# Kernel optimization log

Hardware: AMD Instinct MI355X
Metric: run time of the kernel (lower is better)

The kernel has to match this reference:

```python
import jax, jax.numpy as jnp
import numpy as np

DIM = 768
HEADS = 12

def setup_inputs() -> dict:
    key = jax.random.key(0)
    k_x, k_qw, k_qb, k_pw, k_pb = jax.random.split(key, 5)
    x = jax.random.normal(k_x, (4, 2048, DIM), dtype=jnp.float32)
    s = 1.0 / np.sqrt(DIM)
    # torch nn.Linear convention: y = x @ W.T + b, W shape [out, in]
    qkv_w = jax.random.uniform(k_qw, (3 * DIM, DIM), jnp.float32, -s, s)
    qkv_b = jax.random.uniform(k_qb, (3 * DIM,), jnp.float32, -s, s)
    proj_w = jax.random.uniform(k_pw, (DIM, DIM), jnp.float32, -s, s)
    proj_b = jax.random.uniform(k_pb, (DIM,), jnp.float32, -s, s)
    return {"x": x, "qkv_w": qkv_w, "qkv_b": qkv_b, "proj_w": proj_w, "proj_b": proj_b}

def reference(x, qkv_w, qkv_b, proj_w, proj_b):
    B, N, C = x.shape
    H = HEADS
    D = C // H
    scale = D ** -0.5
    qkv = x @ qkv_w.T + qkv_b                      # [B, N, 3C]
    qkv = qkv.reshape(B, N, 3, H, D).transpose(2, 0, 3, 1, 4)  # [3, B, H, N, D]
    q, k, v = qkv[0], qkv[1], qkv[2]
    attn = jnp.einsum('bhnd,bhmd->bhnm', q, k) * scale  # [B, H, N, N]
    attn = jax.nn.softmax(attn, axis=-1)           # dropout p=0.0 -> identity
    out = jnp.einsum('bhnm,bhmd->bhnd', attn, v)   # [B, H, N, D]
    out = out.transpose(0, 2, 1, 3).reshape(B, N, C)
    return out @ proj_w.T + proj_b
```

## Files before the change

kernel.cpp:

```cpp
#include <hip/hip_runtime.h>

#define DIM 768
#define HEADS 12
#define HDIM 64
#define BATCH 4
#define SEQ 2048
#define QSCALE 0.1803368787f
#define MFIX 16.0f
#define QKVSZ ((size_t)BATCH * HEADS * SEQ * HDIM)

typedef __bf16 bf16x8 __attribute__((ext_vector_type(8)));
typedef float  f32x4  __attribute__((ext_vector_type(4)));
typedef float  f32x16 __attribute__((ext_vector_type(16)));
typedef unsigned short u16x8 __attribute__((ext_vector_type(8)));
typedef unsigned short ushort_t;

__device__ inline float exp2_hw(float x){
    float r;
    asm("v_exp_f32 %0, %1\n\ts_nop 0" : "=v"(r) : "v"(x));
    return r;
}
__device__ inline unsigned short f2bf(float x){
    unsigned int u = __float_as_uint(x);
    u += 0x7fffu + ((u >> 16) & 1u);
    return (unsigned short)(u >> 16);
}
__device__ inline unsigned int cvtpk(float lo, float hi){
    unsigned int r;
    asm("v_cvt_pk_bf16_f32 %0, %1, %2" : "=v"(r) : "v"(lo), "v"(hi));
    return r;
}
__device__ inline void gload_lds16(const void* g, void* lds) {
    __builtin_amdgcn_global_load_lds(
        (const __attribute__((address_space(1))) void*)g,
        (__attribute__((address_space(3))) void*)lds, 16, 0, 0);
}

__global__ __launch_bounds__(256) void cvt3(
    const float* __restrict__ s0, ushort_t* __restrict__ d0, int v0,
    const float* __restrict__ s1, ushort_t* __restrict__ d1, int v1,
    const float* __restrict__ s2, ushort_t* __restrict__ d2, int v2)
{
    int idx = blockIdx.x * 256 + threadIdx.x;
    const float* s; ushort_t* d;
    if (idx < v0)           { s = s0; d = d0; }
    else if (idx < v0 + v1) { idx -= v0; s = s1; d = d1; }
    else                    { idx -= v0 + v1; s = s2; d = d2; }
    float4 a = *(const float4*)(s + (size_t)idx * 8);
    float4 b = *(const float4*)(s + (size_t)idx * 8 + 4);
    u16x8 p;
    p[0] = f2bf(a.x); p[1] = f2bf(a.y); p[2] = f2bf(a.z); p[3] = f2bf(a.w);
    p[4] = f2bf(b.x); p[5] = f2bf(b.y); p[6] = f2bf(b.z); p[7] = f2bf(b.w);
    *(u16x8*)(d + (size_t)idx * 8) = p;
}

template <int MODE>
__global__ __launch_bounds__(256) void gemm_mfma(
    const ushort_t* __restrict__ A, const ushort_t* __restrict__ W,
    const float* __restrict__ bias, void* __restrict__ outp,
    int M, int N, int K)
{
    __shared__ ushort_t As[128 * 64];
    __shared__ ushort_t Bs[128 * 64];

    const int tid  = threadIdx.x;
    const int lane = tid & 63;
    const int w    = tid >> 6;
    const int l16  = lane & 15;
    const int lg   = lane >> 4;
    const int wm = w >> 1, wn = w & 1;
    const int m0 = blockIdx.y << 7;
    const int n0 = blockIdx.x << 7;

    const int srow = lane >> 3;
    const int clds = lane & 7;
    const int cg   = clds ^ srow;
    const ushort_t* pA = A + (size_t)(m0 + w * 32 + srow) * K + cg * 8;
    const ushort_t* pB = W + (size_t)(n0 + w * 32 + srow) * K + cg * 8;
    ushort_t* lA = As + (w * 32) * 64;
    ushort_t* lB = Bs + (w * 32) * 64;

    f32x4 acc[4][4];
#pragma unroll
    for (int mi = 0; mi < 4; ++mi)
#pragma unroll
        for (int ni = 0; ni < 4; ++ni) acc[mi][ni] = (f32x4){0.f, 0.f, 0.f, 0.f};

    const int s7  = l16 & 7;
    const int ck0 = (lg ^ s7) << 3;
    const int ck1 = ((4 | lg) ^ s7) << 3;
    const int arow = (wm * 64 + l16) * 64;
    const int brow = (wn * 64 + l16) * 64;

    const int KT = K >> 6;
    for (int kt = 0; kt < KT; ++kt) {
        __syncthreads();
        const ushort_t* ga = pA + kt * 64;
        const ushort_t* gb = pB + kt * 64;
#pragma unroll
        for (int j = 0; j < 4; ++j) {
            gload_lds16(ga + (size_t)j * 8 * K, lA + j * 8 * 64);
            gload_lds16(gb + (size_t)j * 8 * K, lB + j * 8 * 64);
        }
        __syncthreads();

        bf16x8 af[2][4], bfr[2][4];
#pragma unroll
        for (int mi = 0; mi < 4; ++mi) {
            af[0][mi] = *(const bf16x8*)(As + arow + mi * 16 * 64 + ck0);
            af[1][mi] = *(const bf16x8*)(As + arow + mi * 16 * 64 + ck1);
        }
#pragma unroll
        for (int ni = 0; ni < 4; ++ni) {
            bfr[0][ni] = *(const bf16x8*)(Bs + brow + ni * 16 * 64 + ck0);
            bfr[1][ni] = *(const bf16x8*)(Bs + brow + ni * 16 * 64 + ck1);
        }
#pragma unroll
        for (int kk = 0; kk < 2; ++kk)
#pragma unroll
            for (int mi = 0; mi < 4; ++mi)
#pragma unroll
                for (int ni = 0; ni < 4; ++ni)
                    acc[mi][ni] = __builtin_amdgcn_mfma_f32_16x16x32_bf16(
                        af[kk][mi], bfr[kk][ni], acc[mi][ni], 0, 0, 0);
    }

#pragma unroll
    for (int ni = 0; ni < 4; ++ni) {
        const int n = n0 + wn * 64 + ni * 16 + l16;
        const float bv = bias[n];
        if (MODE == 0) {
            float* out = (float*)outp;
#pragma unroll
            for (int mi = 0; mi < 4; ++mi)
#pragma unroll
                for (int r = 0; r < 4; ++r) {
                    const int m = m0 + wm * 64 + mi * 16 + lg * 4 + r;
                    out[(size_t)m * N + n] = acc[mi][ni][r] + bv;
                }
        } else {
            ushort_t* out = (ushort_t*)outp;
            const int which = n / DIM;
            const int rem   = n % DIM;
            const int h = rem >> 6;
            const int d = rem & 63;
            const float sc = (which == 0) ? QSCALE : 1.0f;
            ushort_t* base = out + (size_t)which * QKVSZ;
#pragma unroll
            for (int mi = 0; mi < 4; ++mi)
#pragma unroll
                for (int r = 0; r < 4; ++r) {
                    const int m = m0 + wm * 64 + mi * 16 + lg * 4 + r;
                    const int b = m >> 11;
                    const int nrow = m & (SEQ - 1);
                    base[((size_t)(b * HEADS + h) * SEQ + nrow) * HDIM + d] =
                        f2bf((acc[mi][ni][r] + bv) * sc);
                }
        }
    }
}

__global__ __launch_bounds__(256) void transpose_v(
    const ushort_t* __restrict__ V, ushort_t* __restrict__ VT)
{
    __shared__ ushort_t t[64][65];
    const int tid = threadIdx.x;
    const int bh  = blockIdx.y;
    const int k0  = blockIdx.x << 6;

#pragma unroll
    for (int p = 0; p < 2; ++p) {
        int idx = tid + (p << 8);
        int row = idx >> 3;
        int ch  = idx & 7;
        union { bf16x8 v; ushort_t s[8]; } u;
        u.v = *(const bf16x8*)(V + ((size_t)bh * SEQ + k0 + row) * HDIM + ch * 8);
#pragma unroll
        for (int j = 0; j < 8; ++j) t[row][ch * 8 + j] = u.s[j];
    }
    __syncthreads();
#pragma unroll
    for (int p = 0; p < 2; ++p) {
        int idx = tid + (p << 8);
        int d   = idx >> 3;
        int ch  = idx & 7;
        union { bf16x8 v; ushort_t s[8]; } u;
#pragma unroll
        for (int j = 0; j < 8; ++j) u.s[j] = t[ch * 8 + j][d];
        *(bf16x8*)(VT + ((size_t)bh * HDIM + d) * SEQ + k0 + ch * 8) = u.v;
    }
}

__global__ __launch_bounds__(256) void flash_attn_mfma(
    const ushort_t* __restrict__ Qg, const ushort_t* __restrict__ Kg,
    const ushort_t* __restrict__ VTg, ushort_t* __restrict__ Og)
{
    __shared__ ushort_t Ks[2][64 * 64];
    __shared__ ushort_t Vs[2][64 * 64];

    const int tid  = threadIdx.x;
    const int lane = tid & 63;
    const int w    = tid >> 6;
    const int l32  = lane & 31;
    const int hi   = lane >> 5;

    const int L   = blockIdx.x;
    const int swz = (L & 7) * 96 + (L >> 3);
    const int bh  = swz >> 4;
    const int qt  = swz & 15;
    const int q0  = qt * 128 + w * 32;

    const ushort_t* Qp  = Qg + ((size_t)bh * SEQ + q0) * HDIM;
    const ushort_t* Kp  = Kg + (size_t)bh * SEQ * HDIM;
    const ushort_t* VTp = VTg + (size_t)bh * HDIM * SEQ;

    bf16x8 qf[4];
#pragma unroll
    for (int kd = 0; kd < 4; ++kd)
        qf[kd] = *(const bf16x8*)(Qp + l32 * HDIM + kd * 16 + hi * 8);

    f32x16 oacc[2];
#pragma unroll
    for (int nb = 0; nb < 2; ++nb)
#pragma unroll
        for (int r = 0; r < 16; ++r) oacc[nb][r] = 0.f;
    float lsum = 0.f;

    const int srow = lane >> 3;
    const int clds = lane & 7;
    const int cg   = clds ^ srow;
    const int rw   = w * 16 + srow;

    auto stage = [&](int buf, int kt) {
        ushort_t* lk = Ks[buf] + w * 1024;
        ushort_t* lv = Vs[buf] + w * 1024;
        const ushort_t* gk = Kp + ((size_t)kt * 64 + rw) * HDIM + cg * 8;
        const ushort_t* gv = VTp + (size_t)rw * SEQ + kt * 64 + cg * 8;
#pragma unroll
        for (int j = 0; j < 2; ++j) {
            gload_lds16(gk + j * 8 * HDIM, lk + j * 512);
            gload_lds16(gv + j * 8 * SEQ,  lv + j * 512);
        }
    };

    stage(0, 0);
    __syncthreads();

    int cur = 0;
    const int NT = SEQ / 64;
    for (int kt = 0; kt < NT; ++kt) {
        if (kt + 1 < NT) stage(cur ^ 1, kt + 1);

        const ushort_t* Kb = Ks[cur];
        const ushort_t* Vb = Vs[cur];

#pragma unroll
        for (int b = 0; b < 2; ++b) {
            f32x16 sacc;
#pragma unroll
            for (int r = 0; r < 16; ++r) sacc[r] = 0.f;
            const int arow = b * 32 + l32;
            const int s7   = arow & 7;
            __builtin_amdgcn_s_setprio(1);
#pragma unroll
            for (int kd = 0; kd < 4; ++kd) {
                bf16x8 kf = *(const bf16x8*)(Kb + arow * 64 + (((kd * 2 + hi) ^ s7) << 3));
                sacc = __builtin_amdgcn_mfma_f32_32x32x16_bf16(kf, qf[kd], sacc, 0, 0, 0);
            }
            __builtin_amdgcn_s_setprio(0);

            float p[16];
#pragma unroll
            for (int r = 0; r < 16; ++r) p[r] = exp2_hw(sacc[r] - MFIX);
            float t0 = (p[0] + p[1]) + (p[2] + p[3]);
            float t1 = (p[4] + p[5]) + (p[6] + p[7]);
            float t2 = (p[8] + p[9]) + (p[10] + p[11]);
            float t3 = (p[12] + p[13]) + (p[14] + p[15]);
            lsum += (t0 + t1) + (t2 + t3);

#pragma unroll
            for (int s = 0; s < 2; ++s) {
                unsigned int x0 = cvtpk(p[8 * s + 0], p[8 * s + 1]);
                unsigned int y0 = cvtpk(p[8 * s + 4], p[8 * s + 5]);
                unsigned int x1 = cvtpk(p[8 * s + 2], p[8 * s + 3]);
                unsigned int y1 = cvtpk(p[8 * s + 6], p[8 * s + 7]);
                asm("v_permlane32_swap_b32 %0, %1" : "+v"(x0), "+v"(y0));
                asm("v_permlane32_swap_b32 %0, %1" : "+v"(x1), "+v"(y1));
                union { bf16x8 v; unsigned int w4[4]; } pa;
                pa.w4[0] = x0; pa.w4[1] = x1; pa.w4[2] = y0; pa.w4[3] = y1;
                const int kc = b * 4 + s * 2 + hi;
                __builtin_amdgcn_s_setprio(1);
#pragma unroll
                for (int nb = 0; nb < 2; ++nb) {
                    int d = nb * 32 + l32;
                    bf16x8 vf = *(const bf16x8*)(Vb + d * 64 + ((kc ^ (d & 7)) << 3));
                    oacc[nb] = __builtin_amdgcn_mfma_f32_32x32x16_bf16(
                        pa.v, vf, oacc[nb], 0, 0, 0);
                }
                __builtin_amdgcn_s_setprio(0);
            }
        }

        __syncthreads();
        cur ^= 1;
    }

    lsum += __shfl_xor(lsum, 32);
    float linv = 1.0f / lsum;
    const int b_ = bh / HEADS;
    const int h_ = bh % HEADS;
    ushort_t* Ob = Og + ((size_t)b_ * SEQ + q0) * DIM + h_ * HDIM;
#pragma unroll
    for (int r = 0; r < 16; ++r) {
        int q = (r & 3) + 8 * (r >> 2) + 4 * hi;
        float li = __shfl(linv, q);
#pragma unroll
        for (int nb = 0; nb < 2; ++nb)
            Ob[(size_t)q * DIM + nb * 32 + l32] = f2bf(oacc[nb][r] * li);
    }
}

extern "C" void kernel_launch(void* const* d_in, const int* in_sizes, int n_in,
                              void* d_out, int out_size, void* d_ws, size_t ws_size,
                              hipStream_t stream)
{
    const float* x      = (const float*)d_in[0];
    const float* qkv_w  = (const float*)d_in[1];
    const float* qkv_b  = (const float*)d_in[2];
    const float* proj_w = (const float*)d_in[3];
    const float* proj_b = (const float*)d_in[4];
    float* out = (float*)d_out;

    ushort_t* qb     = (ushort_t*)d_ws;
    ushort_t* kb     = qb + QKVSZ;
    ushort_t* vb     = qb + 2 * QKVSZ;
    ushort_t* vtb    = qb + 3 * QKVSZ;
    ushort_t* attn   = qb + 4 * QKVSZ;
    ushort_t* xb     = qb + 5 * QKVSZ;
    ushort_t* qkvwb  = xb + QKVSZ;
    ushort_t* projwb = qkvwb + (size_t)3 * DIM * DIM;

    const int M = BATCH * SEQ;
    const int NX  = M * DIM;
    const int NQW = 3 * DIM * DIM;
    const int NPW = DIM * DIM;

    cvt3<<<dim3((NX + NQW + NPW) / (8 * 256)), dim3(256), 0, stream>>>(
        x, xb, NX / 8, qkv_w, qkvwb, NQW / 8, proj_w, projwb, NPW / 8);

    dim3 g1(3 * DIM / 128, M / 128);
    gemm_mfma<1><<<g1, dim3(256), 0, stream>>>(xb, qkvwb, qkv_b, (void*)qb, M, 3 * DIM, DIM);

    transpose_v<<<dim3(SEQ / 64, BATCH * HEADS), dim3(256), 0, stream>>>(vb, vtb);

    flash_attn_mfma<<<dim3(768), dim3(256), 0, stream>>>(qb, kb, vtb, attn);

    dim3 g3(DIM / 128, M / 128);
    gemm_mfma<0><<<g3, dim3(256), 0, stream>>>(attn, projwb, proj_b, (void*)out, M, DIM, DIM);
}
```

Baseline: 155.1 us.

## Fuse V transpose into QKV GEMM epilogue and compute row sums via MFMA

The QKV GEMM epilogue now writes V directly in transposed [B,H,D,N] layout using packed 4-element stores, which removes the separate transpose_v kernel and its extra global round trip. In the attention kernel, the softmax row sum is accumulated with an extra MFMA against a ones vector instead of scalar adds and shuffles, and the fixed max offset is folded into the score accumulator's initial value. Staging pointer arithmetic is also simplified to incremental pointers. The price is one more MFMA per P-tile, and the transposed V stores in the GEMM are strided rather than contiguous.

New measurement: 146.4 us, median of 2. 1.06x faster.

```diff
diff --git a/kernel.cpp b/kernel.cpp
--- a/kernel.cpp
+++ b/kernel.cpp
@@ -144,50 +144,35 @@
             const int rem   = n % DIM;
             const int h = rem >> 6;
             const int d = rem & 63;
-            const float sc = (which == 0) ? QSCALE : 1.0f;
-            ushort_t* base = out + (size_t)which * QKVSZ;
-#pragma unroll
-            for (int mi = 0; mi < 4; ++mi)
-#pragma unroll
-                for (int r = 0; r < 4; ++r) {
-                    const int m = m0 + wm * 64 + mi * 16 + lg * 4 + r;
+            if (which < 2) {
+                const float sc = (which == 0) ? QSCALE : 1.0f;
+                ushort_t* base = out + (size_t)which * QKVSZ;
+#pragma unroll
+                for (int mi = 0; mi < 4; ++mi)
+#pragma unroll
+                    for (int r = 0; r < 4; ++r) {
+                        const int m = m0 + wm * 64 + mi * 16 + lg * 4 + r;
+                        const int b = m >> 11;
+                        const int nrow = m & (SEQ - 1);
+                        base[((size_t)(b * HEADS + h) * SEQ + nrow) * HDIM + d] =
+                            f2bf((acc[mi][ni][r] + bv) * sc);
+                    }
+            } else {
+                ushort_t* base = out + 2 * QKVSZ;
+#pragma unroll
+                for (int mi = 0; mi < 4; ++mi) {
+                    const int m = m0 + wm * 64 + mi * 16 + lg * 4;
                     const int b = m >> 11;
                     const int nrow = m & (SEQ - 1);
-                    base[((size_t)(b * HEADS + h) * SEQ + nrow) * HDIM + d] =
-                        f2bf((acc[mi][ni][r] + bv) * sc);
+                    ushort4 pk;
+                    pk.x = f2bf(acc[mi][ni][0] + bv);
+                    pk.y = f2bf(acc[mi][ni][1] + bv);
+                    pk.z = f2bf(acc[mi][ni][2] + bv);
+                    pk.w = f2bf(acc[mi][ni][3] + bv);
+                    *(ushort4*)&base[((size_t)(b * HEADS + h) * HDIM + d) * SEQ + nrow] = pk;
                 }
-        }
-    }
-}
-
-__global__ __launch_bounds__(256) void transpose_v(
-    const ushort_t* __restrict__ V, ushort_t* __restrict__ VT)
-{
-    __shared__ ushort_t t[64][65];
-    const int tid = threadIdx.x;
-    const int bh  = blockIdx.y;
-    const int k0  = blockIdx.x << 6;
-
-#pragma unroll
-    for (int p = 0; p < 2; ++p) {
-        int idx = tid + (p << 8);
-        int row = idx >> 3;
-        int ch  = idx & 7;
-        union { bf16x8 v; ushort_t s[8]; } u;
-        u.v = *(const bf16x8*)(V + ((size_t)bh * SEQ + k0 + row) * HDIM + ch * 8);
-#pragma unroll
-        for (int j = 0; j < 8; ++j) t[row][ch * 8 + j] = u.s[j];
-    }
-    __syncthreads();
-#pragma unroll
-    for (int p = 0; p < 2; ++p) {
-        int idx = tid + (p << 8);
-        int d   = idx >> 3;
-        int ch  = idx & 7;
-        union { bf16x8 v; ushort_t s[8]; } u;
-#pragma unroll
-        for (int j = 0; j < 8; ++j) u.s[j] = t[ch * 8 + j][d];
-        *(bf16x8*)(VT + ((size_t)bh * HDIM + d) * SEQ + k0 + ch * 8) = u.v;
+            }
+        }
     }
 }
 
@@ -195,8 +180,8 @@
     const ushort_t* __restrict__ Qg, const ushort_t* __restrict__ Kg,
     const ushort_t* __restrict__ VTg, ushort_t* __restrict__ Og)
 {
-    __shared__ ushort_t Ks[2][64 * 64];
-    __shared__ ushort_t Vs[2][64 * 64];
+    __shared__ ushort_t Ks[2][4096];
+    __shared__ ushort_t Vs[2][4096];
 
     const int tid  = threadIdx.x;
     const int lane = tid & 63;
@@ -219,48 +204,62 @@
     for (int kd = 0; kd < 4; ++kd)
         qf[kd] = *(const bf16x8*)(Qp + l32 * HDIM + kd * 16 + hi * 8);
 
-    f32x16 oacc[2];
+    bf16x8 ones;
+    {
+        union { bf16x8 v; unsigned int w4[4]; } u;
+        u.w4[0] = u.w4[1] = u.w4[2] = u.w4[3] = 0x3F803F80u;
+        ones = u.v;
+    }
+
+    f32x16 oacc[2], lacc;
 #pragma unroll
     for (int nb = 0; nb < 2; ++nb)
 #pragma unroll
         for (int r = 0; r < 16; ++r) oacc[nb][r] = 0.f;
-    float lsum = 0.f;
+#pragma unroll
+    for (int r = 0; r < 16; ++r) lacc[r] = 0.f;
 
     const int srow = lane >> 3;
     const int clds = lane & 7;
     const int cg   = clds ^ srow;
     const int rw   = w * 16 + srow;
 
-    auto stage = [&](int buf, int kt) {
-        ushort_t* lk = Ks[buf] + w * 1024;
-        ushort_t* lv = Vs[buf] + w * 1024;
-        const ushort_t* gk = Kp + ((size_t)kt * 64 + rw) * HDIM + cg * 8;
-        const ushort_t* gv = VTp + (size_t)rw * SEQ + kt * 64 + cg * 8;
-#pragma unroll
-        for (int j = 0; j < 2; ++j) {
-            gload_lds16(gk + j * 8 * HDIM, lk + j * 512);
-            gload_lds16(gv + j * 8 * SEQ,  lv + j * 512);
-        }
+    const ushort_t* gk = Kp + (size_t)rw * HDIM + cg * 8;
+    const ushort_t* gv = VTp + (size_t)rw * SEQ + cg * 8;
+    ushort_t* lk0 = &Ks[0][0] + w * 1024;
+    ushort_t* lv0 = &Vs[0][0] + w * 1024;
+
+    auto stage = [&](int buf) {
+        ushort_t* lkb = lk0 + (buf << 12);
+        ushort_t* lvb = lv0 + (buf << 12);
+        gload_lds16(gk, lkb);
+        gload_lds16(gk + 8 * HDIM, lkb + 512);
+        gload_lds16(gv, lvb);
+        gload_lds16(gv + 8 * SEQ, lvb + 512);
     };
 
-    stage(0, 0);
+    stage(0);
+    gk += 64 * HDIM; gv += 64;
     __syncthreads();
 
     int cur = 0;
     const int NT = SEQ / 64;
     for (int kt = 0; kt < NT; ++kt) {
-        if (kt + 1 < NT) stage(cur ^ 1, kt + 1);
-
-        const ushort_t* Kb = Ks[cur];
-        const ushort_t* Vb = Vs[cur];
+        if (kt + 1 < NT) {
+            stage(cur ^ 1);
+            gk += 64 * HDIM; gv += 64;
+        }
+
+        const ushort_t* Kb = &Ks[0][0] + (cur << 12);
+        const ushort_t* Vb = &Vs[0][0] + (cur << 12);
 
 #pragma unroll
         for (int b = 0; b < 2; ++b) {
             f32x16 sacc;
 #pragma unroll
-            for (int r = 0; r < 16; ++r) sacc[r] = 0.f;
+            for (int r = 0; r < 16; ++r) sacc[r] = -MFIX;
             const int arow = b * 32 + l32;
-            const int s7   = arow & 7;
+            const int s7   = l32 & 7;
             __builtin_amdgcn_s_setprio(1);
 #pragma unroll
             for (int kd = 0; kd < 4; ++kd) {
@@ -271,12 +270,7 @@
 
             float p[16];
 #pragma unroll
-            for (int r = 0; r < 16; ++r) p[r] = exp2_hw(sacc[r] - MFIX);
-            float t0 = (p[0] + p[1]) + (p[2] + p[3]);
-            float t1 = (p[4] + p[5]) + (p[6] + p[7]);
-            float t2 = (p[8] + p[9]) + (p[10] + p[11]);
-            float t3 = (p[12] + p[13]) + (p[14] + p[15]);
-            lsum += (t0 + t1) + (t2 + t3);
+            for (int r = 0; r < 16; ++r) p[r] = exp2_hw(sacc[r]);
 
 #pragma unroll
             for (int s = 0; s < 2; ++s) {
@@ -290,6 +284,7 @@
                 pa.w4[0] = x0; pa.w4[1] = x1; pa.w4[2] = y0; pa.w4[3] = y1;
                 const int kc = b * 4 + s * 2 + hi;
                 __builtin_amdgcn_s_setprio(1);
+                lacc = __builtin_amdgcn_mfma_f32_32x32x16_bf16(pa.v, ones, lacc, 0, 0, 0);
 #pragma unroll
                 for (int nb = 0; nb < 2; ++nb) {
                     int d = nb * 32 + l32;
@@ -305,15 +300,13 @@
         cur ^= 1;
     }
 
-    lsum += __shfl_xor(lsum, 32);
-    float linv = 1.0f / lsum;
     const int b_ = bh / HEADS;
     const int h_ = bh % HEADS;
     ushort_t* Ob = Og + ((size_t)b_ * SEQ + q0) * DIM + h_ * HDIM;
 #pragma unroll
     for (int r = 0; r < 16; ++r) {
         int q = (r & 3) + 8 * (r >> 2) + 4 * hi;
-        float li = __shfl(linv, q);
+        float li = __builtin_amdgcn_rcpf(lacc[r]);
 #pragma unroll
         for (int nb = 0; nb < 2; ++nb)
             Ob[(size_t)q * DIM + nb * 32 + l32] = f2bf(oacc[nb][r] * li);
@@ -333,10 +326,9 @@
 
     ushort_t* qb     = (ushort_t*)d_ws;
     ushort_t* kb     = qb + QKVSZ;
-    ushort_t* vb     = qb + 2 * QKVSZ;
-    ushort_t* vtb    = qb + 3 * QKVSZ;
-    ushort_t* attn   = qb + 4 * QKVSZ;
-    ushort_t* xb     = qb + 5 * QKVSZ;
+    ushort_t* vtb    = qb + 2 * QKVSZ;
+    ushort_t* attn   = qb + 3 * QKVSZ;
+    ushort_t* xb     = qb + 4 * QKVSZ;
     ushort_t* qkvwb  = xb + QKVSZ;
     ushort_t* projwb = qkvwb + (size_t)3 * DIM * DIM;
 
@@ -351,8 +343,6 @@
     dim3 g1(3 * DIM / 128, M / 128);
     gemm_mfma<1><<<g1, dim3(256), 0, stream>>>(xb, qkvwb, qkv_b, (void*)qb, M, 3 * DIM, DIM);
 
-    transpose_v<<<dim3(SEQ / 64, BATCH * HEADS), dim3(256), 0, stream>>>(vb, vtb);
-
     flash_attn_mfma<<<dim3(768), dim3(256), 0, stream>>>(qb, kb, vtb, attn);
 
     dim3 g3(DIM / 128, M / 128);
```
